# Kernel tuning notes

Hardware: AMD Instinct MI355X
Metric: run time of the kernel (lower is better)

Reference implementation:

```python
import jax, jax.numpy as jnp
import numpy as np

N, D = 1024, 128
NEG_INF = -1e30


def setup_inputs() -> dict:
    key = jax.random.key(0)
    ks = jax.random.split(key, 8)
    s = 0.05
    return {
        "X": jax.random.normal(ks[0], (N, D), dtype=jnp.float32),
        "Wq": jax.random.normal(ks[1], (D, D), dtype=jnp.float32) * s,
        "Wk": jax.random.normal(ks[2], (D, D), dtype=jnp.float32) * s,
        "v": jax.random.normal(ks[3], (D,), dtype=jnp.float32) * s,
        "w_ih": jax.random.normal(ks[4], (3 * D, 2 * D), dtype=jnp.float32) * s,
        "w_hh": jax.random.normal(ks[5], (3 * D, D), dtype=jnp.float32) * s,
        "b_ih": jax.random.normal(ks[6], (3 * D,), dtype=jnp.float32) * s,
        "b_hh": jax.random.normal(ks[7], (3 * D,), dtype=jnp.float32) * s,
    }


def reference(X, Wq, Wk, v, w_ih, w_hh, b_ih, b_hh):
    n, d = X.shape
    # --- anti-causal additive attention (query i attends keys j >= i) ---
    q = X @ Wq.T                                   # (N, d)
    k = X @ Wk.T                                   # (N, d)
    # scores[i, j] = v . tanh(q_i + k_j)
    scores = jnp.einsum("ijd,d->ij", jnp.tanh(q[:, None, :] + k[None, :, :]), v)
    mask = jnp.arange(n)[None, :] >= jnp.arange(n)[:, None]   # suffix j >= i
    scores = jnp.where(mask, scores, NEG_INF)
    w = jax.nn.softmax(scores, axis=1)             # (N, N)
    att = w @ X                                    # (N, d) context over keys

    # --- single-layer GRU over the N "time" steps, batch 1 ---
    gru_in = jnp.concatenate((X, att), axis=1)     # (N, 2d)
    gi = gru_in @ w_ih.T + b_ih                    # (N, 3d) input gates, precomputed

    def step(h, gi_t):
        gh = h @ w_hh.T + b_hh                     # (3d,)
        i_r, i_z, i_n = jnp.split(gi_t, 3)
        h_r, h_z, h_n = jnp.split(gh, 3)
        r = jax.nn.sigmoid(i_r + h_r)
        z = jax.nn.sigmoid(i_z + h_z)
        nst = jnp.tanh(i_n + r * h_n)
        h_new = (1.0 - z) * nst + z * h
        return h_new, h_new

    h0 = jnp.zeros((d,), dtype=X.dtype)
    _, out = jax.lax.scan(step, h0, gi)            # (N, d)
    return out
```

## Files before the change

kernel.cpp:

```cpp
#include <hip/hip_runtime.h>
#include <hip/hip_bf16.h>

#define N 1024
#define D 128
#define SB 32
#define NSB (N / SB)

typedef __hip_bfloat16 bf16;
typedef __attribute__((ext_vector_type(8))) short bfx8;
typedef __attribute__((ext_vector_type(4))) float fx4;
typedef __attribute__((ext_vector_type(8))) unsigned short u16x8;

__device__ __forceinline__ float b2f(bf16 x) { return __bfloat162float(x); }
__device__ __forceinline__ short f2bf_bits(float x) {
    bf16 b = __float2bfloat16(x);
    return *reinterpret_cast<short*>(&b);
}
__device__ __forceinline__ float bfbits2f(unsigned short u) {
    return __uint_as_float(((unsigned int)u) << 16);
}
__device__ __forceinline__ float fastrcp(float x) { return __builtin_amdgcn_rcpf(x); }

__device__ __forceinline__ float fast_tanh(float x) {
    float e = __expf(2.f * x);
    return 1.f - 2.f * fastrcp(e + 1.f);
}
__device__ __forceinline__ float fast_sigmoid(float x) {
    return fastrcp(1.f + __expf(-x));
}

__device__ __forceinline__ float sel4(fx4 v, int r) {
    float x = (r & 1) ? v[1] : v[0];
    float y = (r & 1) ? v[3] : v[2];
    return (r & 2) ? y : x;
}

__device__ __forceinline__ void async_copy16(const float* g, void* l) {
    __builtin_amdgcn_global_load_lds((const __attribute__((address_space(1))) void*)g,
                                     (__attribute__((address_space(3))) void*)l, 16, 0, 0);
}

__global__ void sniff_kernel(const unsigned short* __restrict__ xu, int* __restrict__ flag) {
    int l = threadIdx.x;
    int cnt = 0;
#pragma unroll
    for (int k = 0; k < 8; ++k) {
        unsigned short u = xu[2 * (l * 8 + k)];
        int e = (u >> 7) & 0xFF;
        cnt += (e >= 96 && e <= 144) ? 1 : 0;
    }
    for (int off = 32; off > 0; off >>= 1) cnt += __shfl_down(cnt, off);
    if (l == 0) *flag = (cnt > 400) ? 1 : 0;
}

struct ConvArgs {
    const void* p[8];
    float* o[8];
    int n[8];
};
__global__ void convert_kernel(ConvArgs A, const int* __restrict__ flag) {
    int seg = blockIdx.y;
    int n = A.n[seg];
    int isbf = *flag;
    const void* p = A.p[seg];
    float* o = A.o[seg];
    for (int i = blockIdx.x * blockDim.x + threadIdx.x; i < n; i += gridDim.x * blockDim.x) {
        float v = isbf ? b2f(((const bf16*)p)[i]) : ((const float*)p)[i];
        o[i] = v;
    }
}

__global__ void qk_kernel(const float* __restrict__ X, const float* __restrict__ Wq,
                          const float* __restrict__ Wk,
                          float* __restrict__ q, float* __restrict__ kT) {
    int i = blockIdx.x & (N - 1);
    bool is_k = blockIdx.x >= N;
    int d = threadIdx.x;
    const float* W = is_k ? Wk : Wq;
    float acc = 0.f;
#pragma unroll 8
    for (int c = 0; c < D; ++c)
        acc += X[i * D + c] * W[d * D + c];
    if (is_k) kT[d * N + i] = acc;
    else      q[i * D + d] = acc;
}

__global__ void scores_kernel(const float* __restrict__ q, const float* __restrict__ kT,
                              const float* __restrict__ v, float* __restrict__ sc) {
    int i = blockIdx.x;
    __shared__ float qs[D];
    __shared__ float vs[D];
    for (int d = threadIdx.x; d < D; d += blockDim.x) {
        qs[d] = q[i * D + d];
        vs[d] = v[d];
    }
    __syncthreads();
    for (int j = i + (int)threadIdx.x; j < N; j += (int)blockDim.x) {
        float s = 0.f;
#pragma unroll 8
        for (int d = 0; d < D; ++d) {
            float x = qs[d] + kT[d * N + j];
            s += vs[d] * fast_tanh(x);
        }
        sc[i * N + j] = s;
    }
}

__global__ void softmax_kernel(float* __restrict__ sc) {
    int i = blockIdx.x;
    int tid = threadIdx.x;
    __shared__ float red[256];
    float sj[4];
    int cnt = 0;
    float m = -1e30f;
    for (int j = i + tid; j < N; j += 256) {
        sj[cnt] = sc[i * N + j];
        m = fmaxf(m, sj[cnt]);
        ++cnt;
    }
    red[tid] = m;
    __syncthreads();
    for (int s = 128; s > 0; s >>= 1) {
        if (tid < s) red[tid] = fmaxf(red[tid], red[tid + s]);
        __syncthreads();
    }
    m = red[0];
    __syncthreads();
    float p[4];
    float l = 0.f;
    for (int it = 0; it < cnt; ++it) {
        p[it] = __expf(sj[it] - m);
        l += p[it];
    }
    red[tid] = l;
    __syncthreads();
    for (int s = 128; s > 0; s >>= 1) {
        if (tid < s) red[tid] += red[tid + s];
        __syncthreads();
    }
    float inv = fastrcp(red[0]);
    for (int j = tid; j < i; j += 256) sc[i * N + j] = 0.f;
    int it2 = 0;
    for (int j = i + tid; j < N; j += 256, ++it2) sc[i * N + j] = p[it2] * inv;
}

__global__ void att_kernel(const float* __restrict__ w, const float* __restrict__ X,
                           float* __restrict__ att) {
    int i = blockIdx.x;
    int d = threadIdx.x;
    float acc = 0.f;
#pragma unroll 4
    for (int j = 0; j < N; ++j)
        acc += w[i * N + j] * X[j * D + d];
    att[i * D + d] = acc;
}

__global__ void gi_kernel(const float* __restrict__ X, const float* __restrict__ att,
                          const float* __restrict__ w_ih, const float* __restrict__ b_ih,
                          float* __restrict__ gi) {
    int i = blockIdx.x;
    int o = threadIdx.x;
    float acc = b_ih[o];
    const float* wr = w_ih + o * (2 * D);
#pragma unroll 8
    for (int c = 0; c < D; ++c) acc += X[i * D + c] * wr[c];
#pragma unroll 8
    for (int c = 0; c < D; ++c) acc += att[i * D + c] * wr[D + c];
    gi[i * 3 * D + o] = acc;
}

__global__ void __launch_bounds__(256, 1) gru_kernel(const float* __restrict__ gi,
                                                     const float* __restrict__ w_hh,
                                                     const float* __restrict__ b_hh,
                                                     void* __restrict__ out,
                                                     const int* __restrict__ flag) {
    __shared__ float gi_lds[2][SB][3 * D];
    __shared__ short hist[SB + 1][D];
    int t = threadIdx.x;
    int w = t >> 6;
    int l = t & 63;
    int q = l >> 4;
    int nn = l & 15;
    int isbf = *flag;

    bfx8 a[3][2][4];
#pragma unroll
    for (int tau = 0; tau < 3; ++tau)
#pragma unroll
        for (int mqi = 0; mqi < 2; ++mqi)
#pragma unroll
            for (int kc = 0; kc < 4; ++kc) {
                int row = 128 * tau + 16 * (2 * w + mqi) + nn;
                int k0 = 32 * kc + 8 * q;
#pragma unroll
                for (int j = 0; j < 8; ++j)
                    a[tau][mqi][kc][j] = f2bf_bits(w_hh[row * D + k0 + j]);
            }

    int rsel = l & 3;
    int mqsel = (l >> 3) & 1;
    int drow = 32 * w + 16 * mqsel + 4 * q + rsel;
    float b_r = b_hh[drow];
    float b_z = b_hh[D + drow];
    float b_n = b_hh[2 * D + drow];
    float h = 0.f;
    bool writer = (l & 4) == 0;

    int fr = 1 + (t >> 3);
    int fc = (t & 7) * 16;

    {
        const float* src = gi + (size_t)0;
        for (int m = 0; m < 12; ++m) {
            int off = (w * 12 + m) * 256;
            async_copy16(src + off + (l << 2), (char*)&gi_lds[0][0][0] + off * 4);
        }
    }

    for (int sb = 0; sb < NSB; ++sb) {
        int cb = sb & 1;
        if (sb == 0) {
            if (t < 64) ((int*)&hist[0][0])[t] = 0;
        } else {
            u16x8 h0 = *(const u16x8*)&hist[fr][fc];
            u16x8 h1 = *(const u16x8*)&hist[fr][fc + 8];
            int orow = (sb - 1) * SB + fr - 1;
            if (isbf) {
                *(u16x8*)((unsigned short*)out + orow * D + fc) = h0;
                *(u16x8*)((unsigned short*)out + orow * D + fc + 8) = h1;
            } else {
                float* op = (float*)out + orow * D + fc;
                fx4 f0, f1, f2, f3;
#pragma unroll
                for (int j = 0; j < 4; ++j) {
                    f0[j] = bfbits2f(h0[j]);     f1[j] = bfbits2f(h0[4 + j]);
                    f2[j] = bfbits2f(h1[j]);     f3[j] = bfbits2f(h1[4 + j]);
                }
                *(fx4*)op = f0; *(fx4*)(op + 4) = f1;
                *(fx4*)(op + 8) = f2; *(fx4*)(op + 12) = f3;
            }
            if (t < 64) ((int*)&hist[0][0])[t] = ((const int*)&hist[SB][0])[t];
        }
        asm volatile("s_waitcnt vmcnt(0) lgkmcnt(0)\ns_barrier" ::: "memory");

        if (sb + 1 < NSB) {
            const float* src = gi + (size_t)(sb + 1) * SB * 3 * D;
            for (int m = 0; m < 12; ++m) {
                int off = (w * 12 + m) * 256;
                async_copy16(src + off + (l << 2), (char*)&gi_lds[cb ^ 1][0][0] + off * 4);
            }
        }

        for (int s = 0; s < SB; ++s) {
            bfx8 b[4];
#pragma unroll
            for (int kc = 0; kc < 4; ++kc)
                b[kc] = *(const bfx8*)&hist[s][32 * kc + 8 * q];
            float gr = gi_lds[cb][s][drow];
            float gz = gi_lds[cb][s][D + drow];
            float gn = gi_lds[cb][s][2 * D + drow];

            fx4 acc[3][2];
#pragma unroll
            for (int tau = 0; tau < 3; ++tau)
#pragma unroll
                for (int mqi = 0; mqi < 2; ++mqi) {
                    fx4 c = {0.f, 0.f, 0.f, 0.f};
#pragma unroll
                    for (int kc = 0; kc < 4; ++kc)
                        c = __builtin_amdgcn_mfma_f32_16x16x32_bf16(a[tau][mqi][kc], b[kc], c, 0, 0, 0);
                    acc[tau][mqi] = c;
                }

            float ar = mqsel ? sel4(acc[0][1], rsel) : sel4(acc[0][0], rsel);
            float az = mqsel ? sel4(acc[1][1], rsel) : sel4(acc[1][0], rsel);
            float an = mqsel ? sel4(acc[2][1], rsel) : sel4(acc[2][0], rsel);
            float rr = fast_sigmoid(gr + ar + b_r);
            float zz = fast_sigmoid(gz + az + b_z);
            float nst = fast_tanh(gn + rr * (an + b_n));
            h = (1.f - zz) * nst + zz * h;
            if (writer) hist[s + 1][drow] = f2bf_bits(h);
            asm volatile("s_waitcnt lgkmcnt(0)\ns_barrier" ::: "memory");
        }
    }
    {
        u16x8 h0 = *(const u16x8*)&hist[fr][fc];
        u16x8 h1 = *(const u16x8*)&hist[fr][fc + 8];
        int orow = (NSB - 1) * SB + fr - 1;
        if (isbf) {
            *(u16x8*)((unsigned short*)out + orow * D + fc) = h0;
            *(u16x8*)((unsigned short*)out + orow * D + fc + 8) = h1;
        } else {
            float* op = (float*)out + orow * D + fc;
            fx4 f0, f1, f2, f3;
#pragma unroll
            for (int j = 0; j < 4; ++j) {
                f0[j] = bfbits2f(h0[j]);     f1[j] = bfbits2f(h0[4 + j]);
                f2[j] = bfbits2f(h1[j]);     f3[j] = bfbits2f(h1[4 + j]);
            }
            *(fx4*)op = f0; *(fx4*)(op + 4) = f1;
            *(fx4*)(op + 8) = f2; *(fx4*)(op + 12) = f3;
        }
    }
}

extern "C" void kernel_launch(void* const* d_in, const int* in_sizes, int n_in,
                              void* d_out, int out_size, void* d_ws, size_t ws_size,
                              hipStream_t stream) {
    (void)in_sizes; (void)n_in; (void)out_size; (void)ws_size;

    float* w0 = (float*)d_ws;
    int*   flag = (int*)w0;
    float* Xf   = w0 + 16;
    float* Wqf  = Xf   + N * D;
    float* Wkf  = Wqf  + D * D;
    float* vf   = Wkf  + D * D;
    float* wihf = vf   + D;
    float* whhf = wihf + 3 * D * 2 * D;
    float* bihf = whhf + 3 * D * D;
    float* bhhf = bihf + 3 * D;
    float* q    = bhhf + 3 * D;
    float* kT   = q    + N * D;
    float* sc   = kT   + N * D;
    float* att  = sc   + (size_t)N * N;
    float* gi   = att  + N * D;

    sniff_kernel<<<1, 64, 0, stream>>>((const unsigned short*)d_in[0], flag);

    ConvArgs A;
    A.p[0] = d_in[0]; A.o[0] = Xf;   A.n[0] = N * D;
    A.p[1] = d_in[1]; A.o[1] = Wqf;  A.n[1] = D * D;
    A.p[2] = d_in[2]; A.o[2] = Wkf;  A.n[2] = D * D;
    A.p[3] = d_in[3]; A.o[3] = vf;   A.n[3] = D;
    A.p[4] = d_in[4]; A.o[4] = wihf; A.n[4] = 3 * D * 2 * D;
    A.p[5] = d_in[5]; A.o[5] = whhf; A.n[5] = 3 * D * D;
    A.p[6] = d_in[6]; A.o[6] = bihf; A.n[6] = 3 * D;
    A.p[7] = d_in[7]; A.o[7] = bhhf; A.n[7] = 3 * D;
    dim3 cgrid(128, 8, 1);
    convert_kernel<<<cgrid, 256, 0, stream>>>(A, flag);

    qk_kernel<<<2 * N, D, 0, stream>>>(Xf, Wqf, Wkf, q, kT);
    scores_kernel<<<N, 256, 0, stream>>>(q, kT, vf, sc);
    softmax_kernel<<<N, 256, 0, stream>>>(sc);
    att_kernel<<<N, D, 0, stream>>>(sc, Xf, att);
    gi_kernel<<<N, 3 * D, 0, stream>>>(Xf, att, wihf, bihf, gi);
    gru_kernel<<<1, 256, 0, stream>>>(gi, whhf, bhhf, d_out, flag);
}
```

Before: 689.6 us.

## Fuse scores, softmax, attention and input-gate GEMM into one kernel; fold GRU bias into MFMA

Merges the scores, softmax, weighted-sum and gi kernels into a single per-row attn_kernel. Softmax weights stay in shared memory, so the N×N score matrix and the att buffer are never written to or read from global memory, and three launches go away. w_ih is transposed once so the gi reads are coalesced. In the GRU loop, b_hh is preloaded as the MFMA accumulator init and pointer increments replace index math, which shortens each serial step; the cost is some extra registers.

```diff
diff --git a/kernel.cpp b/kernel.cpp
--- a/kernel.cpp
+++ b/kernel.cpp
@@ -70,6 +70,13 @@
     }
 }
 
+__global__ void transpose_wih(const float* __restrict__ wih, float* __restrict__ wihT) {
+    int id = blockIdx.x * 256 + threadIdx.x;
+    int c = id / 384;
+    int o = id - c * 384;
+    wihT[id] = wih[o * 256 + c];
+}
+
 __global__ void qk_kernel(const float* __restrict__ X, const float* __restrict__ Wq,
                           const float* __restrict__ Wk,
                           float* __restrict__ q, float* __restrict__ kT) {
@@ -85,88 +92,74 @@
     else      q[i * D + d] = acc;
 }
 
-__global__ void scores_kernel(const float* __restrict__ q, const float* __restrict__ kT,
-                              const float* __restrict__ v, float* __restrict__ sc) {
+__global__ void __launch_bounds__(256) attn_kernel(const float* __restrict__ q,
+                                                   const float* __restrict__ kT,
+                                                   const float* __restrict__ v,
+                                                   const float* __restrict__ X,
+                                                   const float* __restrict__ wihT,
+                                                   const float* __restrict__ b_ih,
+                                                   float* __restrict__ gi) {
     int i = blockIdx.x;
-    __shared__ float qs[D];
-    __shared__ float vs[D];
-    for (int d = threadIdx.x; d < D; d += blockDim.x) {
-        qs[d] = q[i * D + d];
-        vs[d] = v[d];
-    }
-    __syncthreads();
-    for (int j = i + (int)threadIdx.x; j < N; j += (int)blockDim.x) {
-        float s = 0.f;
-#pragma unroll 8
-        for (int d = 0; d < D; ++d) {
-            float x = qs[d] + kT[d * N + j];
-            s += vs[d] * fast_tanh(x);
-        }
-        sc[i * N + j] = s;
-    }
-}
-
-__global__ void softmax_kernel(float* __restrict__ sc) {
-    int i = blockIdx.x;
-    int tid = threadIdx.x;
+    __shared__ float qs[D], vs[D], xr[D], al[D];
+    __shared__ float wrow[N];
     __shared__ float red[256];
+    int t = threadIdx.x;
+    if (t < D) { qs[t] = q[i * D + t]; vs[t] = v[t]; xr[t] = X[i * D + t]; }
+    __syncthreads();
+
     float sj[4];
     int cnt = 0;
     float m = -1e30f;
-    for (int j = i + tid; j < N; j += 256) {
-        sj[cnt] = sc[i * N + j];
-        m = fmaxf(m, sj[cnt]);
-        ++cnt;
-    }
-    red[tid] = m;
-    __syncthreads();
-    for (int s = 128; s > 0; s >>= 1) {
-        if (tid < s) red[tid] = fmaxf(red[tid], red[tid + s]);
+    for (int j = i + t; j < N; j += 256) {
+        float s = 0.f;
+#pragma unroll 8
+        for (int d = 0; d < D; ++d) s += vs[d] * fast_tanh(qs[d] + kT[d * N + j]);
+        sj[cnt++] = s;
+        m = fmaxf(m, s);
+    }
+    red[t] = m;
+    __syncthreads();
+    for (int st = 128; st > 0; st >>= 1) {
+        if (t < st) red[t] = fmaxf(red[t], red[t + st]);
         __syncthreads();
     }
     m = red[0];
     __syncthreads();
-    float p[4];
-    float l = 0.f;
-    for (int it = 0; it < cnt; ++it) {
-        p[it] = __expf(sj[it] - m);
-        l += p[it];
-    }
-    red[tid] = l;
-    __syncthreads();
-    for (int s = 128; s > 0; s >>= 1) {
-        if (tid < s) red[tid] += red[tid + s];
+    float lsum = 0.f;
+    {
+        int it = 0;
+        for (int j = i + t; j < N; j += 256, ++it) {
+            float p = __expf(sj[it] - m);
+            wrow[j] = p;
+            lsum += p;
+        }
+    }
+    red[t] = lsum;
+    __syncthreads();
+    for (int st = 128; st > 0; st >>= 1) {
+        if (t < st) red[t] += red[t + st];
         __syncthreads();
     }
     float inv = fastrcp(red[0]);
-    for (int j = tid; j < i; j += 256) sc[i * N + j] = 0.f;
-    int it2 = 0;
-    for (int j = i + tid; j < N; j += 256, ++it2) sc[i * N + j] = p[it2] * inv;
-}
-
-__global__ void att_kernel(const float* __restrict__ w, const float* __restrict__ X,
-                           float* __restrict__ att) {
-    int i = blockIdx.x;
-    int d = threadIdx.x;
+    __syncthreads();
+
+    int d = t & 127, half = t >> 7;
     float acc = 0.f;
-#pragma unroll 4
-    for (int j = 0; j < N; ++j)
-        acc += w[i * N + j] * X[j * D + d];
-    att[i * D + d] = acc;
-}
-
-__global__ void gi_kernel(const float* __restrict__ X, const float* __restrict__ att,
-                          const float* __restrict__ w_ih, const float* __restrict__ b_ih,
-                          float* __restrict__ gi) {
-    int i = blockIdx.x;
-    int o = threadIdx.x;
-    float acc = b_ih[o];
-    const float* wr = w_ih + o * (2 * D);
+    for (int j = i + half; j < N; j += 2) acc += wrow[j] * X[j * D + d];
+    if (half) red[d] = acc;
+    __syncthreads();
+    if (!half) al[d] = (acc + red[d]) * inv;
+    __syncthreads();
+
+    for (int o = t; o < 3 * D; o += 256) {
+        float a2 = b_ih[o];
+        const float* wt = wihT + o;
 #pragma unroll 8
-    for (int c = 0; c < D; ++c) acc += X[i * D + c] * wr[c];
+        for (int c = 0; c < D; ++c) a2 += xr[c] * wt[c * 384];
 #pragma unroll 8
-    for (int c = 0; c < D; ++c) acc += att[i * D + c] * wr[D + c];
-    gi[i * 3 * D + o] = acc;
+        for (int c = 0; c < D; ++c) a2 += al[c] * wt[(D + c) * 384];
+        gi[i * 3 * D + o] = a2;
+    }
 }
 
 __global__ void __launch_bounds__(256, 1) gru_kernel(const float* __restrict__ gi,
@@ -196,23 +189,27 @@
                 for (int j = 0; j < 8; ++j)
                     a[tau][mqi][kc][j] = f2bf_bits(w_hh[row * D + k0 + j]);
             }
+    fx4 bias[3][2];
+#pragma unroll
+    for (int tau = 0; tau < 3; ++tau)
+#pragma unroll
+        for (int mqi = 0; mqi < 2; ++mqi)
+#pragma unroll
+            for (int r = 0; r < 4; ++r)
+                bias[tau][mqi][r] = b_hh[128 * tau + 16 * (2 * w + mqi) + 4 * q + r];
 
     int rsel = l & 3;
     int mqsel = (l >> 3) & 1;
     int drow = 32 * w + 16 * mqsel + 4 * q + rsel;
-    float b_r = b_hh[drow];
-    float b_z = b_hh[D + drow];
-    float b_n = b_hh[2 * D + drow];
     float h = 0.f;
-    bool writer = (l & 4) == 0;
 
     int fr = 1 + (t >> 3);
     int fc = (t & 7) * 16;
 
     {
-        const float* src = gi + (size_t)0;
-        for (int m = 0; m < 12; ++m) {
-            int off = (w * 12 + m) * 256;
+        const float* src = gi;
+        for (int mm = 0; mm < 12; ++mm) {
+            int off = (w * 12 + mm) * 256;
             async_copy16(src + off + (l << 2), (char*)&gi_lds[0][0][0] + off * 4);
         }
     }
@@ -245,41 +242,50 @@
 
         if (sb + 1 < NSB) {
             const float* src = gi + (size_t)(sb + 1) * SB * 3 * D;
-            for (int m = 0; m < 12; ++m) {
-                int off = (w * 12 + m) * 256;
+            for (int mm = 0; mm < 12; ++mm) {
+                int off = (w * 12 + mm) * 256;
                 async_copy16(src + off + (l << 2), (char*)&gi_lds[cb ^ 1][0][0] + off * 4);
             }
         }
 
+        const char* hrd = (const char*)&hist[0][0] + 16 * q;
+        const float* gp = &gi_lds[cb][0][0] + drow;
+        short* hwr = &hist[1][0] + drow;
+
         for (int s = 0; s < SB; ++s) {
-            bfx8 b[4];
-#pragma unroll
-            for (int kc = 0; kc < 4; ++kc)
-                b[kc] = *(const bfx8*)&hist[s][32 * kc + 8 * q];
-            float gr = gi_lds[cb][s][drow];
-            float gz = gi_lds[cb][s][D + drow];
-            float gn = gi_lds[cb][s][2 * D + drow];
+            bfx8 b0 = *(const bfx8*)(hrd);
+            bfx8 b1 = *(const bfx8*)(hrd + 64);
+            bfx8 b2 = *(const bfx8*)(hrd + 128);
+            bfx8 b3 = *(const bfx8*)(hrd + 192);
+            float gr = gp[0];
+            float gz = gp[D];
+            float gn = gp[2 * D];
 
             fx4 acc[3][2];
 #pragma unroll
             for (int tau = 0; tau < 3; ++tau)
 #pragma unroll
                 for (int mqi = 0; mqi < 2; ++mqi) {
-                    fx4 c = {0.f, 0.f, 0.f, 0.f};
-#pragma unroll
-                    for (int kc = 0; kc < 4; ++kc)
-                        c = __builtin_amdgcn_mfma_f32_16x16x32_bf16(a[tau][mqi][kc], b[kc], c, 0, 0, 0);
+                    fx4 c = bias[tau][mqi];
+                    c = __builtin_amdgcn_mfma_f32_16x16x32_bf16(a[tau][mqi][0], b0, c, 0, 0, 0);
+                    c = __builtin_amdgcn_mfma_f32_16x16x32_bf16(a[tau][mqi][1], b1, c, 0, 0, 0);
+                    c = __builtin_amdgcn_mfma_f32_16x16x32_bf16(a[tau][mqi][2], b2, c, 0, 0, 0);
+                    c = __builtin_amdgcn_mfma_f32_16x16x32_bf16(a[tau][mqi][3], b3, c, 0, 0, 0);
                     acc[tau][mqi] = c;
                 }
 
-            float ar = mqsel ? sel4(acc[0][1], rsel) : sel4(acc[0][0], rsel);
-            float az = mqsel ? sel4(acc[1][1], rsel) : sel4(acc[1][0], rsel);
-            float an = mqsel ? sel4(acc[2][1], rsel) : sel4(acc[2][0], rsel);
-            float rr = fast_sigmoid(gr + ar + b_r);
-            float zz = fast_sigmoid(gz + az + b_z);
-            float nst = fast_tanh(gn + rr * (an + b_n));
+            float ar = sel4(mqsel ? acc[0][1] : acc[0][0], rsel);
+            float az = sel4(mqsel ? acc[1][1] : acc[1][0], rsel);
+            float an = sel4(mqsel ? acc[2][1] : acc[2][0], rsel);
+            float rr = fast_sigmoid(gr + ar);
+            float zz = fast_sigmoid(gz + az);
+            float nst = fast_tanh(gn + rr * an);
             h = (1.f - zz) * nst + zz * h;
-            if (writer) hist[s + 1][drow] = f2bf_bits(h);
+            *hwr = f2bf_bits(h);
+
+            hrd += 256;
+            gp += 3 * D;
+            hwr += D;
             asm volatile("s_waitcnt lgkmcnt(0)\ns_barrier" ::: "memory");
         }
     }
@@ -321,9 +327,8 @@
     float* bhhf = bihf + 3 * D;
     float* q    = bhhf + 3 * D;
     float* kT   = q    + N * D;
-    float* sc   = kT   + N * D;
-    float* att  = sc   + (size_t)N * N;
-    float* gi   = att  + N * D;
+    float* wihT = kT   + N * D;
+    float* gi   = wihT + 3 * D * 2 * D;
 
     sniff_kernel<<<1, 64, 0, stream>>>((const unsigned short*)d_in[0], flag);
 
@@ -339,10 +344,8 @@
     dim3 cgrid(128, 8, 1);
     convert_kernel<<<cgrid, 256, 0, stream>>>(A, flag);
 
+    transpose_wih<<<(3 * D * 2 * D) / 256, 256, 0, stream>>>(wihf, wihT);
     qk_kernel<<<2 * N, D, 0, stream>>>(Xf, Wqf, Wkf, q, kT);
-    scores_kernel<<<N, 256, 0, stream>>>(q, kT, vf, sc);
-    softmax_kernel<<<N, 256, 0, stream>>>(sc);
-    att_kernel<<<N, D, 0, stream>>>(sc, Xf, att);
-    gi_kernel<<<N, 3 * D, 0, stream>>>(Xf, att, wihf, bihf, gi);
+    attn_kernel<<<N, 256, 0, stream>>>(q, kT, vf, Xf, wihT, bihf, gi);
     gru_kernel<<<1, 256, 0, stream>>>(gi, whhf, bhhf, d_out, flag);
 }
```

New measurement: 632.8 us. 1.09x faster.
